# Kernel tuning notes

Hardware: AMD Instinct MI355X
Metric: run time of the kernel (lower is better)

Reference implementation:

```python
import jax, jax.numpy as jnp
import numpy as np


def _solve(f, lmbda, nu, repeats, l):
    h, w, nc = f.shape
    proj = l * (l + 1) // 2
    # enumeration order of (k1,k2) pairs matches the torch double loop
    k1s = np.array([k1 for k1 in range(l) for k2 in range(k1, l)], dtype=np.int32)
    k2s = np.array([k2 for k1 in range(l) for k2 in range(k1, l)], dtype=np.int32)
    zs = np.arange(l)
    # M[p, z] = 1 iff k1s[p] <= z <= k2s[p]  (the k_indices membership)
    M = jnp.asarray(((k1s[:, None] <= zs[None, :]) & (zs[None, :] <= k2s[:, None])).astype(np.float32))
    k1s_j = jnp.asarray(k1s)
    k2s_j = jnp.asarray(k2s)

    sigmap = 1.0 / (3.0 + l)
    sigmas = 1.0
    tauu = 1.0 / 6.0
    tau_mu = 1.0 / (2.0 + proj / 4.0)

    kl = jnp.arange(1, l + 1, dtype=jnp.float32) / l            # k/l, k=1..l
    dist2 = (kl[None, None, None, :] - f[..., None]) ** 2       # (h,w,nc,l)

    def bound(x1, x2):
        return 0.25 * (x1 * x1 + x2 * x2) - lmbda * dist2

    def parabola(p1, p2, p3, ubar, mu1, mu2):
        # forward differences, zero-padded at the far edge
        u1 = jnp.diff(ubar, axis=0, append=ubar[-1:, :, :, :])
        u2 = jnp.diff(ubar, axis=1, append=ubar[:, -1:, :, :])
        u3 = jnp.diff(ubar, axis=3, append=ubar[:, :, :, -1:])
        mu1sum = jnp.einsum('hwcp,pz->hwcz', mu1, M)
        mu2sum = jnp.einsum('hwcp,pz->hwcz', mu2, M)
        u1 = p1 + sigmap * (u1 + mu1sum)
        u2 = p2 + sigmap * (u2 + mu2sum)
        u3 = p3 + sigmap * u3
        B = bound(u1, u2)
        mask = u3 < B
        y = u3 + lmbda * dist2
        norm = jnp.sqrt(u1 * u1 + u2 * u2)
        a = 0.5 * norm                      # 2*0.25*norm
        b = (2.0 / 3.0) * (1.0 - 0.5 * y)   # 2/3*(1 - 2*0.25*y)
        neg_b = b < 0
        sb = jnp.sqrt(jnp.where(neg_b, -b, 1.0))   # sqrt(-b), guarded
        sb3 = sb * sb * sb
        d = jnp.where(neg_b, (a - sb3) * (a + sb3), a * a + b * b * b)
        d_pos = d >= 0
        c = jnp.cbrt(a + jnp.sqrt(jnp.where(d_pos, d, 0.0)))  # a+sqrt(d)>=0
        c_safe = jnp.where(c == 0, 1.0, c)
        ratio = jnp.clip(a / jnp.where(neg_b, sb3, 1.0), -1.0, 1.0)
        v_trig = 2.0 * sb * jnp.cos(jnp.arccos(ratio) / 3.0)
        v = jnp.where(d_pos & (c == 0), 0.0,
                      jnp.where(~d_pos, v_trig, c - b / c_safe))
        norm_safe = jnp.where(norm == 0, 1.0, norm)
        scale = (v / 0.5) / norm_safe       # v/(2*0.25)/norm
        p1n = jnp.where(mask, jnp.where(norm == 0, 0.0, scale * u1), u1)
        p2n = jnp.where(mask, jnp.where(norm == 0, 0.0, scale * u2), u2)
        p3n = jnp.where(mask, bound(p1n, p2n), u3)
        return p1n, p2n, p3n

    def l2proj(s1, s2, mb1, mb2):
        m1 = s1 - sigmas * mb1
        m2 = s2 - sigmas * mb2
        norm = jnp.sqrt(m1 * m1 + m2 * m2)
        mask = norm > nu
        ns = jnp.where(mask, norm, 1.0)
        return jnp.where(mask, m1 * nu / ns, m1), jnp.where(mask, m2 * nu / ns, m2)

    def mu_step(p1, p2, s1, s2, mu1, mu2):
        # interval sums sum_{k=k1..k2} p via exclusive cumsum differences
        zpad = jnp.zeros(p1.shape[:3] + (1,), p1.dtype)
        cs1 = jnp.concatenate([zpad, jnp.cumsum(p1, axis=3)], axis=3)
        cs2 = jnp.concatenate([zpad, jnp.cumsum(p2, axis=3)], axis=3)
        t1 = cs1[..., k2s_j + 1] - cs1[..., k1s_j]
        t2 = cs2[..., k2s_j + 1] - cs2[..., k1s_j]
        mu1n = mu1 + tau_mu * (s1 - t1)
        mu2n = mu2 + tau_mu * (s2 - t2)
        return mu1n, mu2n, 2.0 * mu1n - mu1, 2.0 * mu2n - mu2

    def clipping(p1, p2, p3, u):
        # adjoint (backward) differences of p[:-1] zero-padded on both sides
        z0 = jnp.zeros((1, w, nc, l), u.dtype)
        z1 = jnp.zeros((h, 1, nc, l), u.dtype)
        z3 = jnp.zeros((h, w, nc, 1), u.dtype)
        d1 = jnp.diff(jnp.concatenate([z0, p1[:-1], z0], axis=0), axis=0)
        d2 = jnp.diff(jnp.concatenate([z1, p2[:, :-1], z1], axis=1), axis=1)
        d3 = jnp.diff(jnp.concatenate([z3, p3[..., :-1], z3], axis=3), axis=3)
        un = jnp.clip(u + tauu * (d1 + d2 + d3), 0.0, 1.0)
        un = un.at[..., 0].set(1.0).at[..., l - 1].set(0.0)
        return un, 2.0 * un - u

    u0 = jnp.broadcast_to(f[..., None], (h, w, nc, l)).astype(jnp.float32)
    zl = jnp.zeros((h, w, nc, l), jnp.float32)
    zp = jnp.zeros((h, w, nc, proj), jnp.float32)
    state = (u0, u0, zl, zl, zl, zp, zp, zp, zp, zp, zp, jnp.array(False))

    def body(state, i):
        u, ubar, p1, p2, p3, s1, s2, mu1, mu2, mb1, mb2, done = state
        p1n, p2n, p3n = parabola(p1, p2, p3, ubar, mu1, mu2)
        s1n, s2n = l2proj(s1, s2, mb1, mb2)
        mu1n, mu2n, mb1n, mb2n = mu_step(p1n, p2n, s1n, s2n, mu1, mu2)
        un, ubarn = clipping(p1n, p2n, p3n, u)
        nrj = jnp.sum(jnp.abs(un - u))  # h_u vs h_un
        conv = ((i % 10) == 0) & (nrj / (w * h * l) <= 5e-5)
        keep = lambda old, new: jnp.where(done, old, new)
        new = (keep(u, un), keep(ubar, ubarn), keep(p1, p1n), keep(p2, p2n),
               keep(p3, p3n), keep(s1, s1n), keep(s2, s2n), keep(mu1, mu1n),
               keep(mu2, mu2n), keep(mb1, mb1n), keep(mb2, mb2n), done | conv)
        return new, None

    state, _ = jax.lax.scan(body, state, jnp.arange(repeats))
    return state[0]


def setup_inputs() -> dict:
    key = jax.random.key(0)
    f = jax.random.uniform(key, (384, 384, 1), dtype=jnp.float32)
    return {"f": f, "lmbda": jnp.float32(1.0), "nu": jnp.float32(1.0),
            "repeats": 6, "l": 12}


def reference(f, lmbda, nu, repeats, l):
    return _solve(f, lmbda, nu, repeats, l)
```

## Files before the change

### kernel.cpp

```cpp
#include <hip/hip_runtime.h>
#include <hip/hip_fp16.h>
#include <math.h>

#define H 384
#define W 384
#define NPIX (H * W)
#define L 12
#define REPEATS 6
#define QPS ((size_t)3 * NPIX)

__host__ __device__ constexpr int pbase(int k1) { return k1 * L - (k1 * (k1 - 1)) / 2; }

struct alignas(8) P1 { __half2 mu, d; };

union U4 { uint4 v; unsigned w[4]; };
union U2 { uint2 v; unsigned w[2]; __half h[4]; };

__device__ __forceinline__ __half2 h2bits(unsigned u) {
  union { unsigned u; __half2 h; } c; c.u = u; return c.h;
}
__device__ __forceinline__ unsigned bits_h2(__half2 h) {
  union { unsigned u; __half2 h; } c; c.h = h; return c.u;
}

__device__ __forceinline__ void parabola_proj(float u1, float u2, float u3, float ld2,
                                              float& p1n, float& p2n, float& p3n) {
  const float n2 = u1 * u1 + u2 * u2;
  const float Bb = 0.25f * n2 - ld2;
  const bool mask = u3 < Bb;
  const float y = u3 + ld2;
  const float norm = sqrtf(n2);
  const float a = 0.5f * norm;
  const float b = (2.0f / 3.0f) * (1.0f - 0.5f * y);
  const bool neg_b = b < 0.0f;
  const float sb = sqrtf(neg_b ? -b : 1.0f);
  const float sb3 = sb * sb * sb;
  const float d = neg_b ? (a - sb3) * (a + sb3) : (a * a + b * b * b);
  const bool d_pos = d >= 0.0f;
  const float c = cbrtf(a + sqrtf(d_pos ? d : 0.0f));
  const float c_safe = (c == 0.0f) ? 1.0f : c;
  const float ratio = fminf(fmaxf(a / (neg_b ? sb3 : 1.0f), -1.0f), 1.0f);
  const float v_trig = 2.0f * sb * cosf(acosf(ratio) * (1.0f / 3.0f));
  const float v = (d_pos && c == 0.0f) ? 0.0f
                  : (!d_pos ? v_trig : (c - b / c_safe));
  const float norm_safe = (norm == 0.0f) ? 1.0f : norm;
  const float scale = (2.0f * v) / norm_safe;
  if (mask) {
    p1n = (norm == 0.0f) ? 0.0f : scale * u1;
    p2n = (norm == 0.0f) ? 0.0f : scale * u2;
    p3n = 0.25f * (p1n * p1n + p2n * p2n) - ld2;
  } else {
    p1n = u1; p2n = u2; p3n = u3;
  }
}

__device__ __forceinline__ void load_cs(int pix, const uint4* __restrict__ p12q,
                                        float* cs1, float* cs2) {
  cs1[0] = 0.0f; cs2[0] = 0.0f;
#pragma unroll
  for (int g = 0; g < 3; ++g) {
    U4 v; v.v = p12q[(size_t)g * NPIX + pix];
#pragma unroll
    for (int q = 0; q < 4; ++q) {
      const float2 t = __half22float2(h2bits(v.w[q]));
      const int z = 4 * g + q;
      cs1[z + 1] = cs1[z] + t.x;
      cs2[z + 1] = cs2[z] + t.y;
    }
  }
}

__device__ __forceinline__ float2 pair_adv(float nu, float t1, float t2,
                                           __half2& mu, __half2& d) {
  const float2 dd = __half22float2(d);
  const float n2 = dd.x * dd.x + dd.y * dd.y;
  const float sc = fminf(nu * rsqrtf(n2), 1.0f);
  const float s1 = dd.x * sc, s2 = dd.y * sc;
  const float2 m = __half22float2(mu);
  const float tau = 1.0f / 21.5f;
  const float m1 = m.x + tau * (s1 - t1);
  const float m2 = m.y + tau * (s2 - t2);
  mu = __floats2half2_rn(m1, m2);
  d  = __floats2half2_rn(s1 - 2.0f * m1 + m.x, s2 - 2.0f * m2 + m.y);
  return make_float2(m1, m2);
}

template <int R, bool ACC>
__device__ __forceinline__ void row_step(float nu, const float* cs1, const float* cs2,
                                         P1* st, float* ms1, float* ms2) {
  float r1 = 0.0f, r2 = 0.0f;
#pragma unroll
  for (int k2 = L - 1; k2 >= R; --k2) {
    const float2 m = pair_adv(nu, cs1[k2 + 1] - cs1[R], cs2[k2 + 1] - cs2[R],
                              st[k2 - R].mu, st[k2 - R].d);
    if constexpr (ACC) { r1 += m.x; r2 += m.y; ms1[k2] += r1; ms2[k2] += r2; }
  }
}

template <int KB, int KE, bool LOADCK, bool STORECK, int NTOT,
          int RA, int OA, int RB, int OB, int RC, int OC, int RD, int OD>
__device__ __forceinline__ void replay_worker(int pix, int wkr, float nu,
    const uint4* __restrict__ hist, uint4* __restrict__ ck,
    float* ms1, float* ms2, float* cs1, float* cs2) {
  P1 st[NTOT];
  uint4* ckt = ck + ((size_t)wkr * NPIX + pix) * 10;
  if constexpr (LOADCK) {
#pragma unroll
    for (int s = 0; s < NTOT; s += 2) {
      U4 v; v.v = ckt[s >> 1];
      st[s].mu = h2bits(v.w[0]); st[s].d = h2bits(v.w[1]);
      if (s + 1 < NTOT) { st[s + 1].mu = h2bits(v.w[2]); st[s + 1].d = h2bits(v.w[3]); }
    }
  } else {
    const __half2 z2 = __floats2half2_rn(0.0f, 0.0f);
#pragma unroll
    for (int q = 0; q < NTOT; ++q) { st[q].mu = z2; st[q].d = z2; }
  }

  for (int i = KB; i < KE - 1; ++i) {
    load_cs(pix, hist + (size_t)i * QPS, cs1, cs2);
    row_step<RA, false>(nu, cs1, cs2, st + OA, ms1, ms2);
    if constexpr (RB < 12) row_step<RB, false>(nu, cs1, cs2, st + OB, ms1, ms2);
    if constexpr (RC < 12) row_step<RC, false>(nu, cs1, cs2, st + OC, ms1, ms2);
    if constexpr (RD < 12) row_step<RD, false>(nu, cs1, cs2, st + OD, ms1, ms2);
  }
  load_cs(pix, hist + (size_t)(KE - 1) * QPS, cs1, cs2);
  row_step<RA, true>(nu, cs1, cs2, st + OA, ms1, ms2);
  if constexpr (RB < 12) row_step<RB, true>(nu, cs1, cs2, st + OB, ms1, ms2);
  if constexpr (RC < 12) row_step<RC, true>(nu, cs1, cs2, st + OC, ms1, ms2);
  if constexpr (RD < 12) row_step<RD, true>(nu, cs1, cs2, st + OD, ms1, ms2);

  if constexpr (STORECK) {
#pragma unroll
    for (int s = 0; s < NTOT; s += 2) {
      U4 v;
      v.w[0] = bits_h2(st[s].mu); v.w[1] = bits_h2(st[s].d);
      const int s1i = (s + 1 < NTOT) ? s + 1 : s;
      v.w[2] = bits_h2(st[s1i].mu); v.w[3] = bits_h2(st[s1i].d);
      ckt[s >> 1] = v.v;
    }
  }
}

template <int G, bool LAST>
__device__ __forceinline__ void epilogue(
    int pix, int lane, const float (*sms)[64][25],
    const float* cs1, const float* cs2,
    const uint4* __restrict__ p12cur, const __half* __restrict__ p3,
    uint4* __restrict__ musum, __half* __restrict__ uh,
    float* __restrict__ uout, __half* __restrict__ ubar) {
  const int i = pix / W;
  const int j = pix - i * W;
  const size_t rec = (size_t)G * NPIX + pix;

  U2 uo; uo.v = *reinterpret_cast<const uint2*>(uh + rec * 4);
  float p3prev = (G == 0) ? 0.0f
      : __half2float(p3[((size_t)(G - 1) * NPIX + pix) * 4 + 3]);
  U2 p3q; p3q.v = *reinterpret_cast<const uint2*>(p3 + rec * 4);
  U4 vup, vlf;
  vup.v = make_uint4(0, 0, 0, 0);
  vlf.v = make_uint4(0, 0, 0, 0);
  if (i > 0) vup.v = p12cur[rec - W];
  if (j > 0) vlf.v = p12cur[rec - 1];

  float vn[4], ubn[4];
  U4 msv;
#pragma unroll
  for (int q = 0; q < 4; ++q) {
    const int z = 4 * G + q;
    if constexpr (!LAST) {
      float m1 = 0.0f, m2 = 0.0f;
#pragma unroll
      for (int w = 0; w < 4; ++w) {
        m1 += sms[w][lane][2 * z];
        m2 += sms[w][lane][2 * z + 1];
      }
      msv.w[q] = bits_h2(__floats2half2_rn(m1, m2));
    }
    const float p1o = cs1[z + 1] - cs1[z];
    const float p2o = cs2[z + 1] - cs2[z];
    const float p1up = __half22float2(h2bits(vup.w[q])).x;
    const float p2lf = __half22float2(h2bits(vlf.w[q])).y;
    const float d1 = ((i < H - 1) ? p1o : 0.0f) - p1up;
    const float d2 = ((j < W - 1) ? p2o : 0.0f) - p2lf;
    const float p3c = __half2float(p3q.h[q]);
    const float d3 = ((z < L - 1) ? p3c : 0.0f) - p3prev;
    p3prev = p3c;
    const float uov = __half2float(uo.h[q]);
    float v = fminf(fmaxf(uov + (1.0f / 6.0f) * (d1 + d2 + d3), 0.0f), 1.0f);
    if (z == 0) v = 1.0f;
    if (z == L - 1) v = 0.0f;
    vn[q] = v;
    ubn[q] = 2.0f * v - uov;
  }

  if constexpr (LAST) {
    reinterpret_cast<float4*>(uout)[(size_t)pix * 3 + G] =
        make_float4(vn[0], vn[1], vn[2], vn[3]);
  } else {
    musum[rec] = msv.v;
    U2 uhv, ubv;
    uhv.w[0] = bits_h2(__floats2half2_rn(vn[0], vn[1]));
    uhv.w[1] = bits_h2(__floats2half2_rn(vn[2], vn[3]));
    ubv.w[0] = bits_h2(__floats2half2_rn(ubn[0], ubn[1]));
    ubv.w[1] = bits_h2(__floats2half2_rn(ubn[2], ubn[3]));
    *reinterpret_cast<uint2*>(uh + rec * 4) = uhv.v;
    *reinterpret_cast<uint2*>(ubar + rec * 4) = ubv.v;
  }
}

__global__ __launch_bounds__(256) void k_dual0(
    const float* __restrict__ f, const uint4* __restrict__ hist,
    const __half* __restrict__ p3, __half* __restrict__ uh,
    uint4* __restrict__ musum, __half* __restrict__ ubar) {
  const int pix = blockIdx.x * 256 + threadIdx.x;
  const int i = pix / W;
  const int j = pix - i * W;
  const float tau = 1.0f / 21.5f;
  const float fv = f[pix];

  float cs1[L + 1], cs2[L + 1];
  load_cs(pix, hist, cs1, cs2);

  float suf1 = 0.0f, suf2 = 0.0f;
#pragma unroll
  for (int k = 1; k <= L; ++k) { suf1 += cs1[k]; suf2 += cs2[k]; }
  float pre1 = 0.0f, pre2 = 0.0f;

  float p3prev = 0.0f;
#pragma unroll
  for (int g = 0; g < 3; ++g) {
    const size_t rec = (size_t)g * NPIX + pix;
    U4 vup, vlf;
    vup.v = make_uint4(0, 0, 0, 0);
    vlf.v = make_uint4(0, 0, 0, 0);
    if (i > 0) vup.v = hist[rec - W];
    if (j > 0) vlf.v = hist[rec - 1];
    U2 p3q; p3q.v = *reinterpret_cast<const uint2*>(p3 + rec * 4);
    U4 msv; U2 uhv, ubv;
    float vn[4];
#pragma unroll
    for (int q = 0; q < 4; ++q) {
      const int z = 4 * g + q;
      const float m1 = -tau * ((float)(z + 1) * suf1 - (float)(L - z) * pre1);
      const float m2 = -tau * ((float)(z + 1) * suf2 - (float)(L - z) * pre2);
      suf1 -= cs1[z + 1]; pre1 += cs1[z + 1];
      suf2 -= cs2[z + 1]; pre2 += cs2[z + 1];
      msv.w[q] = bits_h2(__floats2half2_rn(m1, m2));

      const float p1o = cs1[z + 1] - cs1[z];
      const float p2o = cs2[z + 1] - cs2[z];
      const float p1up = __half22float2(h2bits(vup.w[q])).x;
      const float p2lf = __half22float2(h2bits(vlf.w[q])).y;
      const float d1 = ((i < H - 1) ? p1o : 0.0f) - p1up;
      const float d2 = ((j < W - 1) ? p2o : 0.0f) - p2lf;
      const float p3c = __half2float(p3q.h[q]);
      const float d3 = ((z < L - 1) ? p3c : 0.0f) - p3prev;
      p3prev = p3c;
      float v = fminf(fmaxf(fv + (1.0f / 6.0f) * (d1 + d2 + d3), 0.0f), 1.0f);
      if (z == 0) v = 1.0f;
      if (z == L - 1) v = 0.0f;
      vn[q] = v;
    }
    musum[rec] = msv.v;
    uhv.w[0] = bits_h2(__floats2half2_rn(vn[0], vn[1]));
    uhv.w[1] = bits_h2(__floats2half2_rn(vn[2], vn[3]));
    ubv.w[0] = bits_h2(__floats2half2_rn(2.0f * vn[0] - fv, 2.0f * vn[1] - fv));
    ubv.w[1] = bits_h2(__floats2half2_rn(2.0f * vn[2] - fv, 2.0f * vn[3] - fv));
    *reinterpret_cast<uint2*>(uh + rec * 4) = uhv.v;
    *reinterpret_cast<uint2*>(ubar + rec * 4) = ubv.v;
  }
}

template <int KB, int KE, bool LOADCK, bool STORECK, bool LAST>
__global__ __launch_bounds__(256, 3) void k_dual(
    const float* __restrict__ nu_p,
    const uint4* __restrict__ hist, uint4* __restrict__ ck,
    const __half* __restrict__ p3, __half* __restrict__ uh,
    float* __restrict__ uout, uint4* __restrict__ musum,
    __half* __restrict__ ubar) {
  const int lane = threadIdx.x & 63;
  const int wkr  = threadIdx.x >> 6;
  const int pix  = blockIdx.x * 64 + lane;
  const float nu = *nu_p;
  constexpr int KCUR = KE - 1;

  __shared__ float sms[LAST ? 1 : 4][64][25];

  float cs1[L + 1], cs2[L + 1];
  if constexpr (!LAST) {
    float ms1[L], ms2[L];
#pragma unroll
    for (int z = 0; z < L; ++z) { ms1[z] = 0.0f; ms2[z] = 0.0f; }
    switch (wkr) {
      case 0: replay_worker<KB, KE, LOADCK, STORECK, 20, 0,0, 4,12, 12,0, 12,0>(pix, wkr, nu, hist, ck, ms1, ms2, cs1, cs2); break;
      case 1: replay_worker<KB, KE, LOADCK, STORECK, 19, 1,0, 5,11, 11,18, 12,0>(pix, wkr, nu, hist, ck, ms1, ms2, cs1, cs2); break;
      case 2: replay_worker<KB, KE, LOADCK, STORECK, 20, 2,0, 6,10,  8,16, 12,0>(pix, wkr, nu, hist, ck, ms1, ms2, cs1, cs2); break;
      default:replay_worker<KB, KE, LOADCK, STORECK, 19, 3,0, 7, 9,  9,14, 10,17>(pix, wkr, nu, hist, ck, ms1, ms2, cs1, cs2); break;
    }
#pragma unroll
    for (int z = 0; z < L; ++z) {
      sms[wkr][lane][2 * z]     = ms1[z];
      sms[wkr][lane][2 * z + 1] = ms2[z];
    }
    __syncthreads();
  } else {
    if (wkr < 3) load_cs(pix, hist + (size_t)KCUR * QPS, cs1, cs2);
  }

  const uint4* p12cur = hist + (size_t)KCUR * QPS;
  switch (wkr) {
    case 0: epilogue<0, LAST>(pix, lane, sms, cs1, cs2, p12cur, p3, musum, uh, uout, ubar); break;
    case 1: epilogue<1, LAST>(pix, lane, sms, cs1, cs2, p12cur, p3, musum, uh, uout, ubar); break;
    case 2: epilogue<2, LAST>(pix, lane, sms, cs1, cs2, p12cur, p3, musum, uh, uout, ubar); break;
    default: break;
  }
}

template <bool FIRST>
__global__ __launch_bounds__(256) void k_parabola(
    const float* __restrict__ f, const float* __restrict__ lam_p,
    const __half* __restrict__ ubar, const uint4* __restrict__ musum,
    const uint4* __restrict__ p12prev, uint4* __restrict__ p12cur,
    __half* __restrict__ p3) {
  const int pix = blockIdx.x * 256 + threadIdx.x;
  const int g = blockIdx.y;
  const size_t rec = (size_t)g * NPIX + pix;
  const int i = pix / W;
  const int j = pix - i * W;
  const float lam = *lam_p;
  const float fv = f[pix];
  const float sigmap = 1.0f / 15.0f;

  float u1[4], u2[4], u3[4];
  if (FIRST) {
    const float du1 = (i < H - 1) ? (f[pix + W] - fv) : 0.0f;
    const float du2 = (j < W - 1) ? (f[pix + 1] - fv) : 0.0f;
#pragma unroll
    for (int q = 0; q < 4; ++q) {
      u1[q] = sigmap * du1; u2[q] = sigmap * du2; u3[q] = 0.0f;
    }
  } else {
    U2 uo; uo.v = *reinterpret_cast<const uint2*>(ubar + rec * 4);
    float ubv[5];
#pragma unroll
    for (int q = 0; q < 4; ++q) ubv[q] = __half2float(uo.h[q]);
    ubv[4] = (g < 2) ? __half2float(ubar[(rec + NPIX) * 4]) : 0.0f;
    U2 uw, ur;
    uw.v = make_uint2(0, 0); ur.v = make_uint2(0, 0);
    if (i < H - 1) uw.v = *reinterpret_cast<const uint2*>(ubar + (rec + W) * 4);
    if (j < W - 1) ur.v = *reinterpret_cast<const uint2*>(ubar + (rec + 1) * 4);
    U4 msq; msq.v = musum[rec];
    U4 ppq; ppq.v = p12prev[rec];
    U2 p3q; p3q.v = *reinterpret_cast<const uint2*>(p3 + rec * 4);
#pragma unroll
    for (int q = 0; q < 4; ++q) {
      const int z = 4 * g + q;
      const float du1 = (i < H - 1) ? (__half2float(uw.h[q]) - ubv[q]) : 0.0f;
      const float du2 = (j < W - 1) ? (__half2float(ur.h[q]) - ubv[q]) : 0.0f;
      const float du3 = (z < L - 1) ? (ubv[q + 1] - ubv[q]) : 0.0f;
      const float2 ms = __half22float2(h2bits(msq.w[q]));
      const float2 pp = __half22float2(h2bits(ppq.w[q]));
      const float p3v = __half2float(p3q.h[q]);
      u1[q] = pp.x + sigmap * (du1 + ms.x);
      u2[q] = pp.y + sigmap * (du2 + ms.y);
      u3[q] = p3v + sigmap * du3;
    }
  }

  U4 outv; float p3f[4];
#pragma unroll
  for (int q = 0; q < 4; ++q) {
    const int z = 4 * g + q;
    const float kl = (float)(z + 1) * (1.0f / (float)L);
    const float fd = kl - fv;
    const float ld2 = lam * (fd * fd);
    float p1n, p2n, p3n;
    parabola_proj(u1[q], u2[q], u3[q], ld2, p1n, p2n, p3n);
    outv.w[q] = bits_h2(__floats2half2_rn(p1n, p2n));
    p3f[q] = p3n;
  }
  p12cur[rec] = outv.v;
  U2 p3s;
  p3s.w[0] = bits_h2(__floats2half2_rn(p3f[0], p3f[1]));
  p3s.w[1] = bits_h2(__floats2half2_rn(p3f[2], p3f[3]));
  *reinterpret_cast<uint2*>(p3 + rec * 4) = p3s.v;
}

extern "C" void kernel_launch(void* const* d_in, const int* in_sizes, int n_in,
                              void* d_out, int out_size, void* d_ws, size_t ws_size,
                              hipStream_t stream) {
  const float* f   = (const float*)d_in[0];
  const float* lam = (const float*)d_in[1];
  const float* nu  = (const float*)d_in[2];
  float* u = (float*)d_out;

  char* base = (char*)d_ws;
  size_t off = 0;
  auto carve = [&](size_t bytes) -> void* {
    void* p = base + off;
    off += (bytes + 255) & ~size_t(255);
    return p;
  };
  uint4*  hist  = (uint4*)carve(sizeof(uint4) * (size_t)REPEATS * QPS);
  uint4*  ck    = (uint4*)carve(sizeof(uint4) * (size_t)4 * NPIX * 10);
  uint4*  musum = (uint4*)carve(sizeof(uint4) * QPS);
  __half* p3    = (__half*)carve(sizeof(__half) * QPS * 4);
  __half* ubar  = (__half*)carve(sizeof(__half) * QPS * 4);
  __half* uh    = (__half*)carve(sizeof(__half) * QPS * 4);

  const dim3 gA(NPIX / 256, 3);
  const int gB = NPIX / 64;

  k_parabola<true><<<gA, 256, 0, stream>>>(f, lam, ubar, musum, hist, hist, p3);
  k_dual0<<<NPIX / 256, 256, 0, stream>>>(f, hist, p3, uh, musum, ubar);
  k_parabola<false><<<gA, 256, 0, stream>>>(f, lam, ubar, musum, hist + 0 * QPS, hist + 1 * QPS, p3);
  k_dual<0, 2, false, false, false><<<gB, 256, 0, stream>>>(nu, hist, ck, p3, uh, u, musum, ubar);
  k_parabola<false><<<gA, 256, 0, stream>>>(f, lam, ubar, musum, hist + 1 * QPS, hist + 2 * QPS, p3);
  k_dual<0, 3, false, true, false><<<gB, 256, 0, stream>>>(nu, hist, ck, p3, uh, u, musum, ubar);
  k_parabola<false><<<gA, 256, 0, stream>>>(f, lam, ubar, musum, hist + 2 * QPS, hist + 3 * QPS, p3);
  k_dual<3, 4, true, false, false><<<gB, 256, 0, stream>>>(nu, hist, ck, p3, uh, u, musum, ubar);
  k_parabola<false><<<gA, 256, 0, stream>>>(f, lam, ubar, musum, hist + 3 * QPS, hist + 4 * QPS, p3);
  k_dual<3, 5, true, false, false><<<gB, 256, 0, stream>>>(nu, hist, ck, p3, uh, u, musum, ubar);
  k_parabola<false><<<gA, 256, 0, stream>>>(f, lam, ubar, musum, hist + 4 * QPS, hist + 5 * QPS, p3);
  k_dual<5, 6, false, false, true><<<gB, 256, 0, stream>>>(nu, hist, ck, p3, uh, u, musum, ubar);
}
```

Before: 225.6 us.

## Store replay checkpoints planar per pair and double-buffer to skip a replay step

Replay-state checkpoints move from a per-worker interleaved uint4 record to a planar P1 array indexed by pair, so each pixel lane's access is coalesced across the wavefront. The k_dual for iteration 3 now also writes a second checkpoint buffer, which lets the iteration-4 kernel start replay at step 4 rather than re-running step 3. This removes one replay step of recurrent work and makes checkpoint loads contiguous. The cost is an extra checkpoint store in one kernel and a second workspace buffer.

```diff
diff --git a/kernel.cpp b/kernel.cpp
--- a/kernel.cpp
+++ b/kernel.cpp
@@ -97,48 +97,60 @@
   }
 }
 
-template <int KB, int KE, bool LOADCK, bool STORECK, int NTOT,
-          int RA, int OA, int RB, int OB, int RC, int OC, int RD, int OD>
-__device__ __forceinline__ void replay_worker(int pix, int wkr, float nu,
-    const uint4* __restrict__ hist, uint4* __restrict__ ck,
-    float* ms1, float* ms2, float* cs1, float* cs2) {
-  P1 st[NTOT];
-  uint4* ckt = ck + ((size_t)wkr * NPIX + pix) * 10;
+template <int R, int N>
+__device__ __forceinline__ void ck_load(int pix, const P1* __restrict__ ck, P1* st) {
+#pragma unroll
+  for (int q = 0; q < N; ++q) st[q] = ck[(pbase(R) + q) * NPIX + pix];
+}
+template <int R, int N>
+__device__ __forceinline__ void ck_store(int pix, P1* __restrict__ ck, const P1* st) {
+#pragma unroll
+  for (int q = 0; q < N; ++q) ck[(pbase(R) + q) * NPIX + pix] = st[q];
+}
+
+template <int KB, int KE, bool LOADCK, bool STORECK, int RA, int RB, int RC, int RD>
+__device__ __forceinline__ void replay_worker(int pix, float nu,
+    const uint4* __restrict__ hist, const P1* __restrict__ ckL,
+    P1* __restrict__ ckS, float* ms1, float* ms2, float* cs1, float* cs2) {
+  constexpr int NA = 12 - RA;
+  constexpr int NB = (RB < 12) ? 12 - RB : 1;
+  constexpr int NC = (RC < 12) ? 12 - RC : 1;
+  constexpr int ND = (RD < 12) ? 12 - RD : 1;
+  P1 sa[NA], sb[NB], sc_[NC], sd[ND];
   if constexpr (LOADCK) {
-#pragma unroll
-    for (int s = 0; s < NTOT; s += 2) {
-      U4 v; v.v = ckt[s >> 1];
-      st[s].mu = h2bits(v.w[0]); st[s].d = h2bits(v.w[1]);
-      if (s + 1 < NTOT) { st[s + 1].mu = h2bits(v.w[2]); st[s + 1].d = h2bits(v.w[3]); }
-    }
+    ck_load<RA, NA>(pix, ckL, sa);
+    if constexpr (RB < 12) ck_load<RB, NB>(pix, ckL, sb);
+    if constexpr (RC < 12) ck_load<RC, NC>(pix, ckL, sc_);
+    if constexpr (RD < 12) ck_load<RD, ND>(pix, ckL, sd);
   } else {
     const __half2 z2 = __floats2half2_rn(0.0f, 0.0f);
 #pragma unroll
-    for (int q = 0; q < NTOT; ++q) { st[q].mu = z2; st[q].d = z2; }
+    for (int q = 0; q < NA; ++q) { sa[q].mu = z2; sa[q].d = z2; }
+#pragma unroll
+    for (int q = 0; q < NB; ++q) { sb[q].mu = z2; sb[q].d = z2; }
+#pragma unroll
+    for (int q = 0; q < NC; ++q) { sc_[q].mu = z2; sc_[q].d = z2; }
+#pragma unroll
+    for (int q = 0; q < ND; ++q) { sd[q].mu = z2; sd[q].d = z2; }
   }
 
   for (int i = KB; i < KE - 1; ++i) {
     load_cs(pix, hist + (size_t)i * QPS, cs1, cs2);
-    row_step<RA, false>(nu, cs1, cs2, st + OA, ms1, ms2);
-    if constexpr (RB < 12) row_step<RB, false>(nu, cs1, cs2, st + OB, ms1, ms2);
-    if constexpr (RC < 12) row_step<RC, false>(nu, cs1, cs2, st + OC, ms1, ms2);
-    if constexpr (RD < 12) row_step<RD, false>(nu, cs1, cs2, st + OD, ms1, ms2);
+    row_step<RA, false>(nu, cs1, cs2, sa, ms1, ms2);
+    if constexpr (RB < 12) row_step<RB, false>(nu, cs1, cs2, sb, ms1, ms2);
+    if constexpr (RC < 12) row_step<RC, false>(nu, cs1, cs2, sc_, ms1, ms2);
+    if constexpr (RD < 12) row_step<RD, false>(nu, cs1, cs2, sd, ms1, ms2);
   }
   load_cs(pix, hist + (size_t)(KE - 1) * QPS, cs1, cs2);
-  row_step<RA, true>(nu, cs1, cs2, st + OA, ms1, ms2);
-  if constexpr (RB < 12) row_step<RB, true>(nu, cs1, cs2, st + OB, ms1, ms2);
-  if constexpr (RC < 12) row_step<RC, true>(nu, cs1, cs2, st + OC, ms1, ms2);
-  if constexpr (RD < 12) row_step<RD, true>(nu, cs1, cs2, st + OD, ms1, ms2);
-
+  row_step<RA, true>(nu, cs1, cs2, sa, ms1, ms2);
+  if constexpr (RB < 12) row_step<RB, true>(nu, cs1, cs2, sb, ms1, ms2);
+  if constexpr (RC < 12) row_step<RC, true>(nu, cs1, cs2, sc_, ms1, ms2);
+  if constexpr (RD < 12) row_step<RD, true>(nu, cs1, cs2, sd, ms1, ms2);
   if constexpr (STORECK) {
-#pragma unroll
-    for (int s = 0; s < NTOT; s += 2) {
-      U4 v;
-      v.w[0] = bits_h2(st[s].mu); v.w[1] = bits_h2(st[s].d);
-      const int s1i = (s + 1 < NTOT) ? s + 1 : s;
-      v.w[2] = bits_h2(st[s1i].mu); v.w[3] = bits_h2(st[s1i].d);
-      ckt[s >> 1] = v.v;
-    }
+    ck_store<RA, NA>(pix, ckS, sa);
+    if constexpr (RB < 12) ck_store<RB, NB>(pix, ckS, sb);
+    if constexpr (RC < 12) ck_store<RC, NC>(pix, ckS, sc_);
+    if constexpr (RD < 12) ck_store<RD, ND>(pix, ckS, sd);
   }
 }
 
@@ -275,10 +287,10 @@
 template <int KB, int KE, bool LOADCK, bool STORECK, bool LAST>
 __global__ __launch_bounds__(256, 3) void k_dual(
     const float* __restrict__ nu_p,
-    const uint4* __restrict__ hist, uint4* __restrict__ ck,
-    const __half* __restrict__ p3, __half* __restrict__ uh,
-    float* __restrict__ uout, uint4* __restrict__ musum,
-    __half* __restrict__ ubar) {
+    const uint4* __restrict__ hist, const P1* __restrict__ ckL,
+    P1* __restrict__ ckS, const __half* __restrict__ p3,
+    __half* __restrict__ uh, float* __restrict__ uout,
+    uint4* __restrict__ musum, __half* __restrict__ ubar) {
   const int lane = threadIdx.x & 63;
   const int wkr  = threadIdx.x >> 6;
   const int pix  = blockIdx.x * 64 + lane;
@@ -293,10 +305,10 @@
 #pragma unroll
     for (int z = 0; z < L; ++z) { ms1[z] = 0.0f; ms2[z] = 0.0f; }
     switch (wkr) {
-      case 0: replay_worker<KB, KE, LOADCK, STORECK, 20, 0,0, 4,12, 12,0, 12,0>(pix, wkr, nu, hist, ck, ms1, ms2, cs1, cs2); break;
-      case 1: replay_worker<KB, KE, LOADCK, STORECK, 19, 1,0, 5,11, 11,18, 12,0>(pix, wkr, nu, hist, ck, ms1, ms2, cs1, cs2); break;
-      case 2: replay_worker<KB, KE, LOADCK, STORECK, 20, 2,0, 6,10,  8,16, 12,0>(pix, wkr, nu, hist, ck, ms1, ms2, cs1, cs2); break;
-      default:replay_worker<KB, KE, LOADCK, STORECK, 19, 3,0, 7, 9,  9,14, 10,17>(pix, wkr, nu, hist, ck, ms1, ms2, cs1, cs2); break;
+      case 0: replay_worker<KB, KE, LOADCK, STORECK, 0, 4, 12, 12>(pix, nu, hist, ckL, ckS, ms1, ms2, cs1, cs2); break;
+      case 1: replay_worker<KB, KE, LOADCK, STORECK, 1, 5, 11, 12>(pix, nu, hist, ckL, ckS, ms1, ms2, cs1, cs2); break;
+      case 2: replay_worker<KB, KE, LOADCK, STORECK, 2, 6, 8, 12>(pix, nu, hist, ckL, ckS, ms1, ms2, cs1, cs2); break;
+      default:replay_worker<KB, KE, LOADCK, STORECK, 3, 7, 9, 10>(pix, nu, hist, ckL, ckS, ms1, ms2, cs1, cs2); break;
     }
 #pragma unroll
     for (int z = 0; z < L; ++z) {
@@ -403,7 +415,8 @@
     return p;
   };
   uint4*  hist  = (uint4*)carve(sizeof(uint4) * (size_t)REPEATS * QPS);
-  uint4*  ck    = (uint4*)carve(sizeof(uint4) * (size_t)4 * NPIX * 10);
+  P1*     ckA   = (P1*)carve(sizeof(P1) * (size_t)78 * NPIX);
+  P1*     ckB   = (P1*)carve(sizeof(P1) * (size_t)78 * NPIX);
   uint4*  musum = (uint4*)carve(sizeof(uint4) * QPS);
   __half* p3    = (__half*)carve(sizeof(__half) * QPS * 4);
   __half* ubar  = (__half*)carve(sizeof(__half) * QPS * 4);
@@ -415,13 +428,13 @@
   k_parabola<true><<<gA, 256, 0, stream>>>(f, lam, ubar, musum, hist, hist, p3);
   k_dual0<<<NPIX / 256, 256, 0, stream>>>(f, hist, p3, uh, musum, ubar);
   k_parabola<false><<<gA, 256, 0, stream>>>(f, lam, ubar, musum, hist + 0 * QPS, hist + 1 * QPS, p3);
-  k_dual<0, 2, false, false, false><<<gB, 256, 0, stream>>>(nu, hist, ck, p3, uh, u, musum, ubar);
+  k_dual<0, 2, false, false, false><<<gB, 256, 0, stream>>>(nu, hist, ckA, ckA, p3, uh, u, musum, ubar);
   k_parabola<false><<<gA, 256, 0, stream>>>(f, lam, ubar, musum, hist + 1 * QPS, hist + 2 * QPS, p3);
-  k_dual<0, 3, false, true, false><<<gB, 256, 0, stream>>>(nu, hist, ck, p3, uh, u, musum, ubar);
+  k_dual<0, 3, false, true, false><<<gB, 256, 0, stream>>>(nu, hist, ckA, ckA, p3, uh, u, musum, ubar);
   k_parabola<false><<<gA, 256, 0, stream>>>(f, lam, ubar, musum, hist + 2 * QPS, hist + 3 * QPS, p3);
-  k_dual<3, 4, true, false, false><<<gB, 256, 0, stream>>>(nu, hist, ck, p3, uh, u, musum, ubar);
+  k_dual<3, 4, true, true, false><<<gB, 256, 0, stream>>>(nu, hist, ckA, ckB, p3, uh, u, musum, ubar);
   k_parabola<false><<<gA, 256, 0, stream>>>(f, lam, ubar, musum, hist + 3 * QPS, hist + 4 * QPS, p3);
-  k_dual<3, 5, true, false, false><<<gB, 256, 0, stream>>>(nu, hist, ck, p3, uh, u, musum, ubar);
+  k_dual<4, 5, true, false, false><<<gB, 256, 0, stream>>>(nu, hist, ckB, ckB, p3, uh, u, musum, ubar);
   k_parabola<false><<<gA, 256, 0, stream>>>(f, lam, ubar, musum, hist + 4 * QPS, hist + 5 * QPS, p3);
-  k_dual<5, 6, false, false, true><<<gB, 256, 0, stream>>>(nu, hist, ck, p3, uh, u, musum, ubar);
-}
+  k_dual<5, 6, false, false, true><<<gB, 256, 0, stream>>>(nu, hist, ckA, ckA, p3, uh, u, musum, ubar);
+}
```

After: 326.3 us. +44.6%, slower.
